# Optimization experiments

Hardware: AMD Instinct MI355X
Metric: run time of the kernel (lower is better)

The kernel has to match this reference:

```python
import jax, jax.numpy as jnp
import numpy as np

E = 1024   # embedding_dim
H = 16     # heads
W = 1024   # lag / seq length
B = 4      # batch
D = E // H # head dim


def setup_inputs() -> dict:
    key = jax.random.key(0)
    ks = jax.random.split(key, 5)
    scale = E ** -0.5
    return {
        "x":   jax.random.normal(ks[0], (3, B, E, W), dtype=jnp.float32),
        "L_Q": jax.random.normal(ks[1], (E, E), dtype=jnp.float32) * scale,
        "L_K": jax.random.normal(ks[2], (E, E), dtype=jnp.float32) * scale,
        "L_V": jax.random.normal(ks[3], (E, E), dtype=jnp.float32) * scale,
        "M":   jax.random.normal(ks[4], (E, E), dtype=jnp.float32) * (1.0 / (2 * E)) ** 0.5,
        "b":   jnp.zeros((E, 1), dtype=jnp.float32),
    }


def reference(x, L_Q, L_K, L_V, M, b):
    # x: [3, B, E, W] channels-first; x[0]=K input, x[1]=Q input, x[2]=V input
    K = jnp.einsum('ef,bfw->bew', L_K, x[0])
    Q = jnp.einsum('ef,bfw->bew', L_Q, x[1])
    V = jnp.einsum('ef,bfw->bew', L_V, x[2])
    # reshape to [B, H, D, W]
    Kv = K.reshape(B, H, D, W)
    Qv = Q.reshape(B, H, D, W)
    Vv = V.reshape(B, H, D, W)
    # scores[b,h,q,k] = Q_v^T @ K_v
    scores = jnp.einsum('bhdq,bhdk->bhqk', Qv, Kv)
    # causal mask: -inf for q > k (strictly lower triangle), added BEFORE softmax
    q_idx = jnp.arange(W)[:, None]
    k_idx = jnp.arange(W)[None, :]
    mask = jnp.where(q_idx > k_idx, -jnp.inf, 0.0).astype(scores.dtype)
    scores = scores + mask
    # NON-STANDARD: softmax over the QUERY axis (dim=-2), then scale
    attn = jax.nn.softmax(scores, axis=-2) / (E ** 0.5)
    # V_v @ scores: [B,H,D,W] @ [B,H,W,W] -> [B,H,D,W]
    out = jnp.einsum('bhdq,bhqk->bhdk', Vv, attn).reshape(B, E, W)
    # dense: M @ out + b (dropout identity at inference)
    return jnp.einsum('oe,bew->bow', M, out) + b
```

## Files before the change

### kernel.cpp

```cpp
#include <hip/hip_runtime.h>
#include <stdint.h>
#include <math.h>

#define E_DIM 1024
#define W_DIM 1024
#define EW 1048576L

typedef _Float16 h16;
typedef __attribute__((ext_vector_type(8))) _Float16 h8;
typedef __attribute__((ext_vector_type(4))) float f4;

__device__ __forceinline__ void async_copy16(h16* lds, const h16* g) {
    __builtin_amdgcn_global_load_lds(
        (const __attribute__((address_space(1))) void*)g,
        (__attribute__((address_space(3))) void*)lds, 16, 0, 0);
}

__global__ __launch_bounds__(256) void prep(
    const float* __restrict__ x, const float* __restrict__ LK,
    const float* __restrict__ LQ, const float* __restrict__ LV,
    const float* __restrict__ Mw, h16* __restrict__ xt, h16* __restrict__ wh)
{
    __shared__ float Ts[64][65];
    const int z = blockIdx.z;
    const int t = threadIdx.x;
    if (z < 12) {
        const float* src = x + (long)z * EW;
        h16* dst = xt + (long)z * EW;
        const int e0 = blockIdx.y * 64, w0 = blockIdx.x * 64;
        const int r = t >> 4, c4 = (t & 15) * 4;
        #pragma unroll
        for (int p = 0; p < 4; ++p) {
            float4 v = *reinterpret_cast<const float4*>(src + (long)(e0 + r + p * 16) * W_DIM + w0 + c4);
            Ts[c4 + 0][r + p * 16] = v.x;
            Ts[c4 + 1][r + p * 16] = v.y;
            Ts[c4 + 2][r + p * 16] = v.z;
            Ts[c4 + 3][r + p * 16] = v.w;
        }
        __syncthreads();
        #pragma unroll
        for (int p = 0; p < 4; ++p) {
            int wr = r + p * 16;
            union { h16 h[4]; uint2 u; } o;
            o.h[0] = (h16)Ts[wr][c4 + 0];
            o.h[1] = (h16)Ts[wr][c4 + 1];
            o.h[2] = (h16)Ts[wr][c4 + 2];
            o.h[3] = (h16)Ts[wr][c4 + 3];
            *reinterpret_cast<uint2*>(dst + (long)(w0 + wr) * E_DIM + e0 + c4) = o.u;
        }
    } else {
        const float* srcs[4] = {LK, LQ, LV, Mw};
        const float* s = srcs[z - 12];
        h16* o = wh + (long)(z - 12) * EW;
        long base = ((long)(blockIdx.y * 16 + blockIdx.x)) * 1024 + t;
        #pragma unroll
        for (int k = 0; k < 4; ++k) {
            long i = base + k * 256;
            float4 v = reinterpret_cast<const float4*>(s)[i];
            union { h16 h[4]; uint2 u; } u;
            u.h[0] = (h16)v.x; u.h[1] = (h16)v.y; u.h[2] = (h16)v.z; u.h[3] = (h16)v.w;
            reinterpret_cast<uint2*>(o)[i] = u.u;
        }
    }
}

__global__ __launch_bounds__(256) void gemm_proj3(
    const h16* __restrict__ xh, const h16* __restrict__ Wts,
    h16* __restrict__ KQV)
{
    __shared__ h16 As[128 * 64];
    __shared__ h16 Bs[128 * 64];

    const int t = threadIdx.x;
    const int wave = t >> 6, lane = t & 63;
    const int quad = lane >> 4, l16 = lane & 15;

    const int lin = (int)blockIdx.x + ((int)blockIdx.y << 3) + ((int)blockIdx.z << 6);
    const int swz = (lin & 7) * 96 + (lin >> 3);
    const int bx = swz & 7, by = (swz >> 3) & 7, zz = swz >> 6;

    const int m0 = by * 128, n0 = bx * 128;
    const int wm = (wave >> 1) * 64, wn = (wave & 1) * 64;

    const int proj = zz >> 2, bz = zz & 3;
    const h16 *A, *Bt; h16* C;
    if (proj == 0)      { A = xh + bz * EW;       Bt = Wts;          C = KQV + bz * EW; }
    else if (proj == 1) { A = xh + (4 + bz) * EW; Bt = Wts + EW;     C = KQV + (4 + bz) * EW; }
    else                { A = Wts + 2 * EW;       Bt = xh + (8 + bz) * EW; C = KQV + (8 + bz) * EW; }

    f4 acc[4][4] = {};

    for (int k0 = 0; k0 < 1024; k0 += 64) {
        __syncthreads();
        #pragma unroll
        for (int j = 0; j < 4; ++j) {
            int g = j * 256 + t, row = g >> 3, cg = (g & 7) ^ (row & 7);
            async_copy16(&As[g * 8], A  + (long)(m0 + row) * E_DIM + k0 + cg * 8);
            async_copy16(&Bs[g * 8], Bt + (long)(n0 + row) * E_DIM + k0 + cg * 8);
        }
        __syncthreads();

        h8 av[4][2], bv[4][2];
        #pragma unroll
        for (int i = 0; i < 4; ++i) {
            int ra = wm + i * 16 + l16, rb = wn + i * 16 + l16;
            #pragma unroll
            for (int c = 0; c < 2; ++c) {
                av[i][c] = *reinterpret_cast<const h8*>(&As[(ra * 8 + ((c * 4 + quad) ^ (l16 & 7))) * 8]);
                bv[i][c] = *reinterpret_cast<const h8*>(&Bs[(rb * 8 + ((c * 4 + quad) ^ (l16 & 7))) * 8]);
            }
        }
        #pragma unroll
        for (int c = 0; c < 2; ++c)
            #pragma unroll
            for (int mt = 0; mt < 4; ++mt)
                #pragma unroll
                for (int nt = 0; nt < 4; ++nt)
                    acc[mt][nt] = __builtin_amdgcn_mfma_f32_16x16x32_f16(av[mt][c], bv[nt][c], acc[mt][nt], 0, 0, 0);
    }

    #pragma unroll
    for (int mt = 0; mt < 4; ++mt)
        #pragma unroll
        for (int i = 0; i < 4; ++i) {
            int m = m0 + wm + mt * 16 + quad * 4 + i;
            #pragma unroll
            for (int nt = 0; nt < 4; ++nt)
                C[(long)m * W_DIM + n0 + wn + nt * 16 + l16] = (h16)acc[mt][nt][i];
        }
}

__global__ __launch_bounds__(256) void gemm_out(
    const h16* __restrict__ A, const h16* __restrict__ Bt,
    float* __restrict__ C, const float* __restrict__ bias)
{
    __shared__ h16 As[64 * 64];
    __shared__ h16 Bs[128 * 64];

    const int t = threadIdx.x;
    const int wave = t >> 6, lane = t & 63;
    const int quad = lane >> 4, l16 = lane & 15;
    const int m0 = blockIdx.y * 64, n0 = blockIdx.x * 128;
    const int wm = (wave >> 1) * 32, wn = (wave & 1) * 64;

    f4 acc[2][4] = {};

    for (int k0 = 0; k0 < 1024; k0 += 64) {
        __syncthreads();
        #pragma unroll
        for (int j = 0; j < 2; ++j) {
            int g = j * 256 + t, row = g >> 3, cg = (g & 7) ^ (row & 7);
            async_copy16(&As[g * 8], A + (long)(m0 + row) * E_DIM + k0 + cg * 8);
        }
        #pragma unroll
        for (int j = 0; j < 4; ++j) {
            int g = j * 256 + t, row = g >> 3, cg = (g & 7) ^ (row & 7);
            async_copy16(&Bs[g * 8], Bt + (long)(n0 + row) * E_DIM + k0 + cg * 8);
        }
        __syncthreads();

        h8 av[2][2], bv[4][2];
        #pragma unroll
        for (int c = 0; c < 2; ++c) {
            #pragma unroll
            for (int mt = 0; mt < 2; ++mt) {
                int r = wm + mt * 16 + l16;
                av[mt][c] = *reinterpret_cast<const h8*>(&As[(r * 8 + ((c * 4 + quad) ^ (l16 & 7))) * 8]);
            }
            #pragma unroll
            for (int nt = 0; nt < 4; ++nt) {
                int r = wn + nt * 16 + l16;
                bv[nt][c] = *reinterpret_cast<const h8*>(&Bs[(r * 8 + ((c * 4 + quad) ^ (l16 & 7))) * 8]);
            }
        }
        #pragma unroll
        for (int c = 0; c < 2; ++c)
            #pragma unroll
            for (int mt = 0; mt < 2; ++mt)
                #pragma unroll
                for (int nt = 0; nt < 4; ++nt)
                    acc[mt][nt] = __builtin_amdgcn_mfma_f32_16x16x32_f16(av[mt][c], bv[nt][c], acc[mt][nt], 0, 0, 0);
    }

    #pragma unroll
    for (int mt = 0; mt < 2; ++mt)
        #pragma unroll
        for (int i = 0; i < 4; ++i) {
            int m = m0 + wm + mt * 16 + quad * 4 + i;
            float bv_ = bias ? bias[m] : 0.f;
            #pragma unroll
            for (int nt = 0; nt < 4; ++nt) {
                int n = n0 + wn + nt * 16 + l16;
                C[(long)(n >> 10) * EW + (long)m * W_DIM + (n & 1023)] = acc[mt][nt][i] + bv_;
            }
        }
}

__global__ __launch_bounds__(512) void attn_mfma(
    const h16* __restrict__ Kt, const h16* __restrict__ Qt,
    const h16* __restrict__ V, h16* __restrict__ AoT)
{
    __shared__ h16 Qs[2][64 * 64];
    __shared__ h16 Vs[2][64 * 64];
    __shared__ h16 Ps[8][16 * 64];

    const int t = threadIdx.x, wave = t >> 6, lane = t & 63;
    const int quad = lane >> 4, l16 = lane & 15;
    const int y = blockIdx.y;
    const int b = y >> 4, h = y & 15;
    const int cxor = (y & 7) ^ (((y >> 5) & 1) ? 7 : 0);
    const int ktb = (int)blockIdx.x ^ cxor;
    const int nit = 2 * ktb + 2;
    const int kwave = ktb * 128 + wave * 16;
    const int kc = kwave + l16;

    const h16* Ktb_ = Kt + (long)b * EW + h * 64;
    const h16* Qtb  = Qt + (long)b * EW + h * 64;
    const h16* Vb   = V  + (long)b * EW + (long)(h * 64) * W_DIM;
    h16* Pw = &Ps[wave][0];

    h8 kb0 = *reinterpret_cast<const h8*>(Ktb_ + (long)kc * E_DIM + quad * 8);
    h8 kb1 = *reinterpret_cast<const h8*>(Ktb_ + (long)kc * E_DIM + 32 + quad * 8);

    {
        int row = t >> 3, cg = (t & 7) ^ (row & 7);
        async_copy16(&Qs[0][t * 8], Qtb + (long)row * E_DIM + cg * 8);
        async_copy16(&Vs[0][t * 8], Vb + (long)row * W_DIM + cg * 8);
    }

    const float L2E = 1.442695041f;
    float mr = -1e30f, ls = 0.f;
    f4 O[4] = {};

    for (int it = 0; it < nit; ++it) {
        const int q0 = it * 64;
        __syncthreads();
        if (it + 1 < nit) {
            const int nb = (it + 1) & 1, q1 = q0 + 64;
            int row = t >> 3, cg = (t & 7) ^ (row & 7);
            async_copy16(&Qs[nb][t * 8], Qtb + (long)(q1 + row) * E_DIM + cg * 8);
            async_copy16(&Vs[nb][t * 8], Vb + (long)row * W_DIM + q1 + cg * 8);
        }
        if (q0 > kwave + 15) continue;

        const h16* qs = Qs[it & 1];
        const h16* vs = Vs[it & 1];

        f4 S[4];
        __builtin_amdgcn_s_setprio(1);
        #pragma unroll
        for (int nt = 0; nt < 4; ++nt) {
            int row = nt * 16 + l16;
            h8 a0 = *reinterpret_cast<const h8*>(&qs[(row * 8 + (quad ^ (l16 & 7))) * 8]);
            h8 a1 = *reinterpret_cast<const h8*>(&qs[(row * 8 + ((4 + quad) ^ (l16 & 7))) * 8]);
            f4 s = {};
            s = __builtin_amdgcn_mfma_f32_16x16x32_f16(a0, kb0, s, 0, 0, 0);
            s = __builtin_amdgcn_mfma_f32_16x16x32_f16(a1, kb1, s, 0, 0, 0);
            S[nt] = s;
        }
        __builtin_amdgcn_s_setprio(0);

        if (it >= 2 * ktb) {
            #pragma unroll
            for (int nt = 0; nt < 4; ++nt)
                #pragma unroll
                for (int i = 0; i < 4; ++i)
                    if (q0 + nt * 16 + quad * 4 + i > kc) S[nt][i] = -1e30f;
        }

        float mx = -1e30f;
        #pragma unroll
        for (int nt = 0; nt < 4; ++nt) {
            float t0 = fmaxf(fmaxf(S[nt][0], S[nt][1]), fmaxf(S[nt][2], S[nt][3]));
            mx = fmaxf(mx, t0);
        }
        mx = fmaxf(mx, __shfl_xor(mx, 16));
        mx = fmaxf(mx, __shfl_xor(mx, 32));

        if (__any(mx - mr > 8.f)) {
            float nm = fmaxf(mr, mx);
            float al = exp2f((mr - nm) * L2E);
            mr = nm;
            ls *= al;
            #pragma unroll
            for (int dt = 0; dt < 4; ++dt)
                #pragma unroll
                for (int i = 0; i < 4; ++i) O[dt][i] *= al;
        }

        const float mc = mr * L2E;
        float tsa = 0.f, tsb = 0.f;
        #pragma unroll
        for (int nt = 0; nt < 4; ++nt)
            #pragma unroll
            for (int i = 0; i < 4; ++i) {
                float p = exp2f(fmaf(S[nt][i], L2E, -mc));
                S[nt][i] = p;
                if (i & 1) tsb += p; else tsa += p;
            }
        float ts = tsa + tsb;
        ts += __shfl_xor(ts, 16);
        ts += __shfl_xor(ts, 32);
        ls += ts;

        #pragma unroll
        for (int nt = 0; nt < 4; ++nt) {
            int sg = ((nt * 2 + (quad >> 1)) ^ (l16 & 7)) * 8 + (quad & 1) * 4;
            union { h16 hh[4]; uint2 u2; } u0;
            #pragma unroll
            for (int i = 0; i < 4; ++i) u0.hh[i] = (h16)S[nt][i];
            *reinterpret_cast<uint2*>(Pw + l16 * 64 + sg) = u0.u2;
        }
        asm volatile("" ::: "memory");

        __builtin_amdgcn_s_setprio(1);
        #pragma unroll
        for (int c = 0; c < 2; ++c) {
            int sg = ((c * 4 + quad) ^ (l16 & 7)) * 8;
            h8 pb = *reinterpret_cast<const h8*>(Pw + l16 * 64 + sg);
            #pragma unroll
            for (int dt = 0; dt < 4; ++dt) {
                int r = dt * 16 + l16;
                h8 va = *reinterpret_cast<const h8*>(&vs[(r * 8 + ((c * 4 + quad) ^ (l16 & 7))) * 8]);
                O[dt] = __builtin_amdgcn_mfma_f32_16x16x32_f16(va, pb, O[dt], 0, 0, 0);
            }
        }
        __builtin_amdgcn_s_setprio(0);
    }

    const float inv = 0.03125f / ls;
    #pragma unroll
    for (int dt = 0; dt < 4; ++dt) {
        int sg = ((dt * 2 + (quad >> 1)) ^ (l16 & 7)) * 8 + (quad & 1) * 4;
        union { h16 hh[4]; uint2 u2; } u0;
        #pragma unroll
        for (int i = 0; i < 4; ++i) u0.hh[i] = (h16)(O[dt][i] * inv);
        *reinterpret_cast<uint2*>(Pw + l16 * 64 + sg) = u0.u2;
    }
    asm volatile("" ::: "memory");
    #pragma unroll
    for (int j = 0; j < 2; ++j) {
        int sg = ((quad * 2 + j) ^ (l16 & 7)) * 8;
        uint4 vv = *reinterpret_cast<const uint4*>(Pw + l16 * 64 + sg);
        *reinterpret_cast<uint4*>(AoT + (long)b * EW + (long)(kwave + l16) * E_DIM
                                  + h * 64 + quad * 16 + j * 8) = vv;
    }
}

extern "C" void kernel_launch(void* const* d_in, const int* in_sizes, int n_in,
                              void* d_out, int out_size, void* d_ws, size_t ws_size,
                              hipStream_t stream)
{
    const float* x  = (const float*)d_in[0];
    const float* LQ = (const float*)d_in[1];
    const float* LK = (const float*)d_in[2];
    const float* LV = (const float*)d_in[3];
    const float* Mw = (const float*)d_in[4];
    const float* bb = (const float*)d_in[5];
    float* out = (float*)d_out;
    h16* ws = (h16*)d_ws;

    h16* xh  = ws;
    h16* LKh = ws + 12 * EW;
    h16* Mh  = ws + 15 * EW;
    h16* Kp  = ws + 16 * EW;
    h16* Qp  = ws + 20 * EW;
    h16* Vp  = ws + 24 * EW;
    h16* Ao  = ws + 28 * EW;

    dim3 blk(256);
    prep<<<dim3(16, 16, 16), blk, 0, stream>>>(x, LK, LQ, LV, Mw, xh, LKh);
    gemm_proj3<<<dim3(8, 8, 12), blk, 0, stream>>>(xh, LKh, Kp);
    attn_mfma<<<dim3(8, 64), dim3(512), 0, stream>>>(Kp, Qp, Vp, Ao);
    gemm_out<<<dim3(32, 16), blk, 0, stream>>>(Mh, Ao, out, bb);
}
```

Baseline: 190.8 us.

## Double-buffer projection GEMM with 256x256 tiles and 512-thread blocks

```diff
diff --git a/kernel.cpp b/kernel.cpp
--- a/kernel.cpp
+++ b/kernel.cpp
@@ -64,23 +64,24 @@
     }
 }
 
-__global__ __launch_bounds__(256) void gemm_proj3(
+__global__ __launch_bounds__(512) void gemm_proj3(
     const h16* __restrict__ xh, const h16* __restrict__ Wts,
     h16* __restrict__ KQV)
 {
-    __shared__ h16 As[128 * 64];
-    __shared__ h16 Bs[128 * 64];
+    __shared__ h16 As[2][256 * 64];
+    __shared__ h16 Bs[2][256 * 64];
 
     const int t = threadIdx.x;
     const int wave = t >> 6, lane = t & 63;
     const int quad = lane >> 4, l16 = lane & 15;
-
-    const int lin = (int)blockIdx.x + ((int)blockIdx.y << 3) + ((int)blockIdx.z << 6);
-    const int swz = (lin & 7) * 96 + (lin >> 3);
-    const int bx = swz & 7, by = (swz >> 3) & 7, zz = swz >> 6;
-
-    const int m0 = by * 128, n0 = bx * 128;
-    const int wm = (wave >> 1) * 64, wn = (wave & 1) * 64;
+    const int mi = wave >> 2, ni = wave & 3;
+    const int wm = mi * 128, wn = ni * 64;
+
+    const int lin = (int)blockIdx.x + ((int)blockIdx.y << 2) + ((int)blockIdx.z << 4);
+    const int swz = (lin & 7) * 24 + (lin >> 3);
+    const int bx = swz & 3, by = (swz >> 2) & 3, zz = swz >> 4;
+
+    const int m0 = by * 256, n0 = bx * 256;
 
     const int proj = zz >> 2, bz = zz & 3;
     const h16 *A, *Bt; h16* C;
@@ -88,39 +89,61 @@
     else if (proj == 1) { A = xh + (4 + bz) * EW; Bt = Wts + EW;     C = KQV + (4 + bz) * EW; }
     else                { A = Wts + 2 * EW;       Bt = xh + (8 + bz) * EW; C = KQV + (8 + bz) * EW; }
 
-    f4 acc[4][4] = {};
-
-    for (int k0 = 0; k0 < 1024; k0 += 64) {
-        __syncthreads();
+    f4 acc[8][4] = {};
+
+    auto stage = [&](int buf, int k0) {
         #pragma unroll
         for (int j = 0; j < 4; ++j) {
-            int g = j * 256 + t, row = g >> 3, cg = (g & 7) ^ (row & 7);
-            async_copy16(&As[g * 8], A  + (long)(m0 + row) * E_DIM + k0 + cg * 8);
-            async_copy16(&Bs[g * 8], Bt + (long)(n0 + row) * E_DIM + k0 + cg * 8);
-        }
-        __syncthreads();
-
-        h8 av[4][2], bv[4][2];
-        #pragma unroll
-        for (int i = 0; i < 4; ++i) {
-            int ra = wm + i * 16 + l16, rb = wn + i * 16 + l16;
-            #pragma unroll
-            for (int c = 0; c < 2; ++c) {
-                av[i][c] = *reinterpret_cast<const h8*>(&As[(ra * 8 + ((c * 4 + quad) ^ (l16 & 7))) * 8]);
-                bv[i][c] = *reinterpret_cast<const h8*>(&Bs[(rb * 8 + ((c * 4 + quad) ^ (l16 & 7))) * 8]);
-            }
-        }
-        #pragma unroll
-        for (int c = 0; c < 2; ++c)
-            #pragma unroll
-            for (int mt = 0; mt < 4; ++mt)
-                #pragma unroll
-                for (int nt = 0; nt < 4; ++nt)
-                    acc[mt][nt] = __builtin_amdgcn_mfma_f32_16x16x32_f16(av[mt][c], bv[nt][c], acc[mt][nt], 0, 0, 0);
+            int g = j * 512 + t, row = g >> 3, cg = (g & 7) ^ (row & 7);
+            async_copy16(&As[buf][g * 8], A  + (long)(m0 + row) * E_DIM + k0 + cg * 8);
+            async_copy16(&Bs[buf][g * 8], Bt + (long)(n0 + row) * E_DIM + k0 + cg * 8);
+        }
+    };
+
+    stage(0, 0);
+
+    for (int T = 0; T < 16; ++T) {
+        if (T + 1 < 16) {
+            stage((T + 1) & 1, (T + 1) * 64);
+            asm volatile("s_waitcnt vmcnt(8)" ::: "memory");
+        } else {
+            asm volatile("s_waitcnt vmcnt(0)" ::: "memory");
+        }
+        __builtin_amdgcn_s_barrier();
+
+        const h16* as = As[T & 1];
+        const h16* bs = Bs[T & 1];
+
+        #pragma unroll
+        for (int c = 0; c < 2; ++c) {
+            h8 bv[4];
+            #pragma unroll
+            for (int j = 0; j < 4; ++j) {
+                int rb = wn + j * 16 + l16;
+                bv[j] = *reinterpret_cast<const h8*>(&bs[(rb * 8 + ((c * 4 + quad) ^ (l16 & 7))) * 8]);
+            }
+            #pragma unroll
+            for (int fh = 0; fh < 2; ++fh) {
+                h8 av[4];
+                #pragma unroll
+                for (int i = 0; i < 4; ++i) {
+                    int ra = wm + fh * 64 + i * 16 + l16;
+                    av[i] = *reinterpret_cast<const h8*>(&as[(ra * 8 + ((c * 4 + quad) ^ (l16 & 7))) * 8]);
+                }
+                __builtin_amdgcn_s_setprio(1);
+                #pragma unroll
+                for (int i = 0; i < 4; ++i)
+                    #pragma unroll
+                    for (int j = 0; j < 4; ++j)
+                        acc[fh * 4 + i][j] = __builtin_amdgcn_mfma_f32_16x16x32_f16(av[i], bv[j], acc[fh * 4 + i][j], 0, 0, 0);
+                __builtin_amdgcn_s_setprio(0);
+            }
+        }
+        __builtin_amdgcn_s_barrier();
     }
 
     #pragma unroll
-    for (int mt = 0; mt < 4; ++mt)
+    for (int mt = 0; mt < 8; ++mt)
         #pragma unroll
         for (int i = 0; i < 4; ++i) {
             int m = m0 + wm + mt * 16 + quad * 4 + i;
@@ -370,7 +393,7 @@
 
     dim3 blk(256);
     prep<<<dim3(16, 16, 16), blk, 0, stream>>>(x, LK, LQ, LV, Mw, xh, LKh);
-    gemm_proj3<<<dim3(8, 8, 12), blk, 0, stream>>>(xh, LKh, Kp);
+    gemm_proj3<<<dim3(4, 4, 12), dim3(512), 0, stream>>>(xh, LKh, Kp);
     attn_mfma<<<dim3(8, 64), dim3(512), 0, stream>>>(Kp, Qp, Vp, Ao);
     gemm_out<<<dim3(32, 16), blk, 0, stream>>>(Mh, Ao, out, bb);
 }
```

After: 190.8 us. Within noise of the previous version (+0.0%).
